# Performance work log

Hardware: AMD Instinct MI355X
Metric: run time of the kernel (lower is better)

The kernel has to match this reference:

```python
import jax, jax.numpy as jnp
import numpy as np

B, S, H = 16, 8192, 512

def setup_inputs() -> dict:
    key = jax.random.key(0)
    k1, k2, k3, k4, k5 = jax.random.split(key, 5)
    scale = 1.0 / np.sqrt(H)
    return {
        "encoder_outputs": jax.random.normal(k1, (B, S, H), dtype=jnp.float32),
        "query": jax.random.normal(k2, (B, H), dtype=jnp.float32),
        "W_h": jax.random.normal(k3, (H, H), dtype=jnp.float32) * scale,
        "W_q": jax.random.normal(k4, (H, H), dtype=jnp.float32) * scale,
        "v": jax.random.normal(k5, (H,), dtype=jnp.float32) * scale,
    }

def reference(encoder_outputs, query, W_h, W_q, v):
    # h_proj: (B,S,H) = enc @ W_h^T (torch Linear convention)
    h_proj = jnp.einsum('bsh,oh->bso', encoder_outputs, W_h)
    # q_proj: (B,1,H)
    q_proj = jnp.einsum('bh,oh->bo', query, W_q)[:, None, :]
    # scores: (B,S) = tanh(h_proj + q_proj) @ v
    scores = jnp.einsum('bso,o->bs', jnp.tanh(h_proj + q_proj), v)
    alpha = jax.nn.softmax(scores, axis=1)          # (B,S)
    context = jnp.einsum('bs,bsh->bh', alpha, encoder_outputs)  # (B,H)
    return (context, alpha)
```

## Files before the change

kernel.cpp:

```cpp
#include <hip/hip_runtime.h>

typedef float  f32x4  __attribute__((ext_vector_type(4)));
typedef __bf16 bf16x8 __attribute__((ext_vector_type(8)));

#define LOG2E      1.4426950408889634f
#define TWO_LOG2E  2.8853900817779268f

__device__ __forceinline__ float fast_tanh(float x) {
    float e = __builtin_amdgcn_exp2f(x * TWO_LOG2E);
    return 1.0f - 2.0f * __builtin_amdgcn_rcpf(e + 1.0f);
}

__device__ __forceinline__ int a_chunk(int m, int k8) {
    return (((m >> 4) * 16 + (k8 >> 2)) << 6) +
           ((((k8 & 3) << 4) | (m & 15)) ^ ((k8 >> 2) & 7) ^ (((k8 & 3) << 1) & 7));
}

__global__ void wh_swizzle_kernel(const float* __restrict__ Wh,
                                  __bf16* __restrict__ Wswz) {
    int gid = blockIdx.x * 256 + threadIdx.x;
    int n   = gid >> 6;
    int k8  = gid & 63;
    const float* g = Wh + ((long)n << 9) + (k8 << 3);
    f32x4 f0 = *(const f32x4*)g;
    f32x4 f1 = *(const f32x4*)(g + 4);
    bf16x8 val;
    val[0] = (__bf16)f0[0]; val[1] = (__bf16)f0[1];
    val[2] = (__bf16)f0[2]; val[3] = (__bf16)f0[3];
    val[4] = (__bf16)f1[0]; val[5] = (__bf16)f1[1];
    val[6] = (__bf16)f1[2]; val[7] = (__bf16)f1[3];
    int chunk = (((n >> 4) * 16 + (k8 >> 2)) << 6) + (((k8 & 3) << 4) | (n & 15));
    *(bf16x8*)(Wswz + ((long)chunk << 3)) = val;
}

__global__ void qproj_kernel(const float* __restrict__ query,
                             const float* __restrict__ Wq,
                             float* __restrict__ qp) {
    int pair = (blockIdx.x << 2) + (threadIdx.x >> 6);
    int l    = threadIdx.x & 63;
    int b    = pair >> 9;
    long o   = pair & 511;
    const f32x4* q  = (const f32x4*)(query + (b << 9) + (l << 3));
    const f32x4* wr = (const f32x4*)(Wq + (o << 9) + (l << 3));
    f32x4 a0 = q[0], a1 = q[1], w0 = wr[0], w1 = wr[1];
    float acc = a0[0]*w0[0] + a0[1]*w0[1] + a0[2]*w0[2] + a0[3]*w0[3]
              + a1[0]*w1[0] + a1[1]*w1[1] + a1[2]*w1[2] + a1[3]*w1[3];
    #pragma unroll
    for (int off = 1; off < 64; off <<= 1) acc += __shfl_xor(acc, off, 64);
    if (l == 0) qp[pair] = acc;
}

__global__ __launch_bounds__(512, 4) void score_ctx_kernel(
    const float*  __restrict__ enc,
    const __bf16* __restrict__ Wswz,
    const float*  __restrict__ qp,
    const float*  __restrict__ v,
    float* __restrict__ alpha_out,
    float* __restrict__ ctx_acc,
    float* __restrict__ denom)
{
    __shared__ __align__(16) unsigned char ldsA[65536];
    __shared__ float score_lds[512];
    __shared__ float escore[64];

    const int  t    = threadIdx.x;
    const int  w    = t >> 6;
    const int  l    = t & 63;
    const long row0 = (long)blockIdx.x << 6;
    const int  b    = (int)(row0 >> 13);

    f32x4 acc[4][4];
    float vv[4];
    #pragma unroll
    for (int nt = 0; nt < 4; ++nt) {
        int n = (w << 6) + (nt << 4) + (l & 15);
        float q = qp[(b << 9) + n];
        vv[nt] = v[n];
        f32x4 qv = {q, q, q, q};
        #pragma unroll
        for (int mt = 0; mt < 4; ++mt) acc[nt][mt] = qv;
    }

    #pragma unroll
    for (int i = 0; i < 8; ++i) {
        int cflat = t + (i << 9);
        int m = cflat >> 6, k8 = cflat & 63;
        const float* g = enc + ((row0 + m) << 9) + (k8 << 3);
        f32x4 f0 = *(const f32x4*)g;
        f32x4 f1 = *(const f32x4*)(g + 4);
        bf16x8 val;
        val[0] = (__bf16)f0[0]; val[1] = (__bf16)f0[1];
        val[2] = (__bf16)f0[2]; val[3] = (__bf16)f0[3];
        val[4] = (__bf16)f1[0]; val[5] = (__bf16)f1[1];
        val[6] = (__bf16)f1[2]; val[7] = (__bf16)f1[3];
        *(bf16x8*)(ldsA + (a_chunk(m, k8) << 4)) = val;
    }

    __syncthreads();

    const bf16x8* Bg = (const bf16x8*)Wswz;
    #pragma unroll 2
    for (int s = 0; s < 16; ++s) {
        bf16x8 af[4];
        int lowr = l ^ (s & 7) ^ (((l >> 4) << 1) & 7);
        #pragma unroll
        for (int mt = 0; mt < 4; ++mt)
            af[mt] = *(const bf16x8*)(ldsA + (((((mt << 4) + s) << 6) + lowr) << 4));
        #pragma unroll
        for (int nt = 0; nt < 4; ++nt) {
            bf16x8 bf = Bg[((((w << 2) + nt) * 16 + s) << 6) + l];
            #pragma unroll
            for (int mt = 0; mt < 4; ++mt)
                acc[nt][mt] = __builtin_amdgcn_mfma_f32_16x16x32_bf16(
                    af[mt], bf, acc[nt][mt], 0, 0, 0);
        }
    }

    float srow[16];
    #pragma unroll
    for (int i = 0; i < 16; ++i) srow[i] = 0.f;
    #pragma unroll
    for (int nt = 0; nt < 4; ++nt) {
        float vn = vv[nt];
        #pragma unroll
        for (int mt = 0; mt < 4; ++mt)
            #pragma unroll
            for (int r = 0; r < 4; ++r)
                srow[mt * 4 + r] += vn * fast_tanh(acc[nt][mt][r]);
    }
    #pragma unroll
    for (int i = 0; i < 16; ++i) {
        #pragma unroll
        for (int off = 1; off < 16; off <<= 1)
            srow[i] += __shfl_xor(srow[i], off, 64);
    }
    if ((l & 15) == 0) {
        int qd = l >> 4;
        #pragma unroll
        for (int mt = 0; mt < 4; ++mt)
            #pragma unroll
            for (int r = 0; r < 4; ++r)
                score_lds[(w << 6) + (mt << 4) + (qd << 2) + r] = srow[mt * 4 + r];
    }
    __syncthreads();

    if (t < 64) {
        float sc = 0.f;
        #pragma unroll
        for (int ww = 0; ww < 8; ++ww) sc += score_lds[(ww << 6) + t];
        float e = __builtin_amdgcn_exp2f(sc * LOG2E);
        alpha_out[row0 + t] = e;
        escore[t] = e;
        float ssum = e;
        #pragma unroll
        for (int off = 1; off < 64; off <<= 1) ssum += __shfl_xor(ssum, off, 64);
        if (t == 0) atomicAdd(denom + b, ssum);
    }
    __syncthreads();

    float ca[8];
    #pragma unroll
    for (int j = 0; j < 8; ++j) ca[j] = 0.f;
    #pragma unroll
    for (int ii = 0; ii < 8; ++ii) {
        int m = (w << 3) + ii;
        float em = escore[m];
        bf16x8 av = *(const bf16x8*)(ldsA + (a_chunk(m, l) << 4));
        #pragma unroll
        for (int j = 0; j < 8; ++j) ca[j] += em * (float)av[j];
    }
    __syncthreads();
    float* part = (float*)ldsA;
    #pragma unroll
    for (int j = 0; j < 8; ++j) part[t * 9 + j] = ca[j];
    __syncthreads();
    {
        int h = t;
        int k8h = h >> 3, j = h & 7;
        float sum = 0.f;
        #pragma unroll
        for (int rg = 0; rg < 8; ++rg) sum += part[((rg << 6) | k8h) * 9 + j];
        atomicAdd(ctx_acc + ((long)b << 9) + h, sum);
    }
}

__global__ void normalize_kernel(const float* __restrict__ ctx_acc,
                                 const float* __restrict__ denom,
                                 float* __restrict__ out) {
    int i = blockIdx.x * 256 + threadIdx.x;
    if (i < 8192) {
        int b = i >> 9;
        out[i] = ctx_acc[i] / denom[b];
    } else if (i < 8192 + 131072) {
        int b = (i - 8192) >> 13;
        out[i] = out[i] / denom[b];
    }
}

extern "C" void kernel_launch(void* const* d_in, const int* in_sizes, int n_in,
                              void* d_out, int out_size, void* d_ws, size_t ws_size,
                              hipStream_t stream) {
    const float* enc   = (const float*)d_in[0];
    const float* query = (const float*)d_in[1];
    const float* Wh    = (const float*)d_in[2];
    const float* Wq    = (const float*)d_in[3];
    const float* v     = (const float*)d_in[4];
    float* out = (float*)d_out;

    char* ws = (char*)d_ws;
    float*  ctx_acc = (float*)ws;
    float*  denom   = (float*)(ws + 32768);
    float*  qp      = (float*)(ws + 32832);
    __bf16* Wswz    = (__bf16*)(ws + 65600);

    hipMemsetAsync(ws, 0, 32832, stream);
    wh_swizzle_kernel<<<128, 256, 0, stream>>>(Wh, Wswz);
    qproj_kernel<<<2048, 256, 0, stream>>>(query, Wq, qp);
    score_ctx_kernel<<<2048, 512, 0, stream>>>(enc, Wswz, qp, v,
                                               out + 8192, ctx_acc, denom);
    normalize_kernel<<<544, 256, 0, stream>>>(ctx_acc, denom, out);
}
```

Baseline: 424.2 us.

## Merge prolog kernels, double the block size, and software-pipeline MFMA operand loads

The memset, Wh swizzle and q-projection launches are folded into a single prolog kernel, removing two launches. The score kernel now uses 1024 threads, so each wave covers 32 output columns instead of 64, which halves the accumulator registers. The K loop is software-pipelined: the next LDS A fragments and the B fragments two steps ahead are loaded while the current MFMAs run. The context partial sums gain an extra LDS reduction pass. With launch_bounds(1024,4) and 64KB of LDS per block, fewer blocks can be resident and register pressure is tighter.

```diff
diff --git a/kernel.cpp b/kernel.cpp
--- a/kernel.cpp
+++ b/kernel.cpp
@@ -16,41 +16,50 @@
            ((((k8 & 3) << 4) | (m & 15)) ^ ((k8 >> 2) & 7) ^ (((k8 & 3) << 1) & 7));
 }
 
-__global__ void wh_swizzle_kernel(const float* __restrict__ Wh,
-                                  __bf16* __restrict__ Wswz) {
-    int gid = blockIdx.x * 256 + threadIdx.x;
-    int n   = gid >> 6;
-    int k8  = gid & 63;
-    const float* g = Wh + ((long)n << 9) + (k8 << 3);
-    f32x4 f0 = *(const f32x4*)g;
-    f32x4 f1 = *(const f32x4*)(g + 4);
-    bf16x8 val;
-    val[0] = (__bf16)f0[0]; val[1] = (__bf16)f0[1];
-    val[2] = (__bf16)f0[2]; val[3] = (__bf16)f0[3];
-    val[4] = (__bf16)f1[0]; val[5] = (__bf16)f1[1];
-    val[6] = (__bf16)f1[2]; val[7] = (__bf16)f1[3];
-    int chunk = (((n >> 4) * 16 + (k8 >> 2)) << 6) + (((k8 & 3) << 4) | (n & 15));
-    *(bf16x8*)(Wswz + ((long)chunk << 3)) = val;
-}
-
-__global__ void qproj_kernel(const float* __restrict__ query,
-                             const float* __restrict__ Wq,
-                             float* __restrict__ qp) {
-    int pair = (blockIdx.x << 2) + (threadIdx.x >> 6);
-    int l    = threadIdx.x & 63;
-    int b    = pair >> 9;
-    long o   = pair & 511;
-    const f32x4* q  = (const f32x4*)(query + (b << 9) + (l << 3));
-    const f32x4* wr = (const f32x4*)(Wq + (o << 9) + (l << 3));
-    f32x4 a0 = q[0], a1 = q[1], w0 = wr[0], w1 = wr[1];
-    float acc = a0[0]*w0[0] + a0[1]*w0[1] + a0[2]*w0[2] + a0[3]*w0[3]
-              + a1[0]*w1[0] + a1[1]*w1[1] + a1[2]*w1[2] + a1[3]*w1[3];
-    #pragma unroll
-    for (int off = 1; off < 64; off <<= 1) acc += __shfl_xor(acc, off, 64);
-    if (l == 0) qp[pair] = acc;
-}
-
-__global__ __launch_bounds__(512, 4) void score_ctx_kernel(
+__global__ void prolog_kernel(const float* __restrict__ Wh,
+                              __bf16* __restrict__ Wswz,
+                              const float* __restrict__ query,
+                              const float* __restrict__ Wq,
+                              float* __restrict__ qp,
+                              float* __restrict__ ctx_acc,
+                              float* __restrict__ denom) {
+    const int bid = blockIdx.x;
+    const int t   = threadIdx.x;
+    if (bid < 128) {
+        int gid = (bid << 8) + t;
+        int n   = gid >> 6;
+        int k8  = gid & 63;
+        const float* g = Wh + ((long)n << 9) + (k8 << 3);
+        f32x4 f0 = *(const f32x4*)g;
+        f32x4 f1 = *(const f32x4*)(g + 4);
+        bf16x8 val;
+        val[0] = (__bf16)f0[0]; val[1] = (__bf16)f0[1];
+        val[2] = (__bf16)f0[2]; val[3] = (__bf16)f0[3];
+        val[4] = (__bf16)f1[0]; val[5] = (__bf16)f1[1];
+        val[6] = (__bf16)f1[2]; val[7] = (__bf16)f1[3];
+        int chunk = (((n >> 4) * 16 + (k8 >> 2)) << 6) + (((k8 & 3) << 4) | (n & 15));
+        *(bf16x8*)(Wswz + ((long)chunk << 3)) = val;
+    } else if (bid < 2176) {
+        int pair = ((bid - 128) << 2) + (t >> 6);
+        int l    = t & 63;
+        int b    = pair >> 9;
+        long o   = pair & 511;
+        const f32x4* q  = (const f32x4*)(query + (b << 9) + (l << 3));
+        const f32x4* wr = (const f32x4*)(Wq + (o << 9) + (l << 3));
+        f32x4 a0 = q[0], a1 = q[1], w0 = wr[0], w1 = wr[1];
+        float acc = a0[0]*w0[0] + a0[1]*w0[1] + a0[2]*w0[2] + a0[3]*w0[3]
+                  + a1[0]*w1[0] + a1[1]*w1[1] + a1[2]*w1[2] + a1[3]*w1[3];
+        #pragma unroll
+        for (int off = 1; off < 64; off <<= 1) acc += __shfl_xor(acc, off, 64);
+        if (l == 0) qp[pair] = acc;
+    } else {
+        int i = ((bid - 2176) << 8) + t;
+        if (i < 8192)      ctx_acc[i] = 0.f;
+        else if (i < 8208) denom[i - 8192] = 0.f;
+    }
+}
+
+__global__ __launch_bounds__(1024, 4) void score_ctx_kernel(
     const float*  __restrict__ enc,
     const __bf16* __restrict__ Wswz,
     const float*  __restrict__ qp,
@@ -60,7 +69,7 @@
     float* __restrict__ denom)
 {
     __shared__ __align__(16) unsigned char ldsA[65536];
-    __shared__ float score_lds[512];
+    __shared__ float score_lds[1024];
     __shared__ float escore[64];
 
     const int  t    = threadIdx.x;
@@ -69,11 +78,11 @@
     const long row0 = (long)blockIdx.x << 6;
     const int  b    = (int)(row0 >> 13);
 
-    f32x4 acc[4][4];
-    float vv[4];
-    #pragma unroll
-    for (int nt = 0; nt < 4; ++nt) {
-        int n = (w << 6) + (nt << 4) + (l & 15);
+    f32x4 acc[2][4];
+    float vv[2];
+    #pragma unroll
+    for (int nt = 0; nt < 2; ++nt) {
+        int n = (w << 5) + (nt << 4) + (l & 15);
         float q = qp[(b << 9) + n];
         vv[nt] = v[n];
         f32x4 qv = {q, q, q, q};
@@ -82,9 +91,9 @@
     }
 
     #pragma unroll
-    for (int i = 0; i < 8; ++i) {
-        int cflat = t + (i << 9);
-        int m = cflat >> 6, k8 = cflat & 63;
+    for (int i = 0; i < 4; ++i) {
+        int m  = (t >> 6) + (i << 4);
+        int k8 = t & 63;
         const float* g = enc + ((row0 + m) << 9) + (k8 << 3);
         f32x4 f0 = *(const f32x4*)g;
         f32x4 f1 = *(const f32x4*)(g + 4);
@@ -96,23 +105,44 @@
         *(bf16x8*)(ldsA + (a_chunk(m, k8) << 4)) = val;
     }
 
-    __syncthreads();
-
     const bf16x8* Bg = (const bf16x8*)Wswz;
-    #pragma unroll 2
+    const int j0 = w << 1;
+    bf16x8 bfr[2][2];
+    #pragma unroll
+    for (int nt = 0; nt < 2; ++nt) {
+        bfr[0][nt] = Bg[(((j0 + nt) << 4) + 0 << 6) + l];
+        bfr[1][nt] = Bg[((((j0 + nt) << 4) + 1) << 6) + l];
+    }
+
+    __syncthreads();
+
+    bf16x8 af[2][4];
+    {
+        int lowr = l ^ 0 ^ (((l >> 4) << 1) & 7);
+        #pragma unroll
+        for (int mt = 0; mt < 4; ++mt)
+            af[0][mt] = *(const bf16x8*)(ldsA + ((((mt << 4) << 6) + lowr) << 4));
+    }
+    #pragma unroll
     for (int s = 0; s < 16; ++s) {
-        bf16x8 af[4];
-        int lowr = l ^ (s & 7) ^ (((l >> 4) << 1) & 7);
-        #pragma unroll
-        for (int mt = 0; mt < 4; ++mt)
-            af[mt] = *(const bf16x8*)(ldsA + (((((mt << 4) + s) << 6) + lowr) << 4));
-        #pragma unroll
-        for (int nt = 0; nt < 4; ++nt) {
-            bf16x8 bf = Bg[((((w << 2) + nt) * 16 + s) << 6) + l];
+        const int cur = s & 1, nxt = cur ^ 1;
+        if (s < 15) {
+            int lowr = l ^ ((s + 1) & 7) ^ (((l >> 4) << 1) & 7);
+            #pragma unroll
+            for (int mt = 0; mt < 4; ++mt)
+                af[nxt][mt] = *(const bf16x8*)(
+                    ldsA + (((((mt << 4) + s + 1) << 6) + lowr) << 4));
+        }
+        #pragma unroll
+        for (int nt = 0; nt < 2; ++nt)
             #pragma unroll
             for (int mt = 0; mt < 4; ++mt)
                 acc[nt][mt] = __builtin_amdgcn_mfma_f32_16x16x32_bf16(
-                    af[mt], bf, acc[nt][mt], 0, 0, 0);
+                    af[cur][mt], bfr[cur][nt], acc[nt][mt], 0, 0, 0);
+        if (s + 2 < 16) {
+            #pragma unroll
+            for (int nt = 0; nt < 2; ++nt)
+                bfr[cur][nt] = Bg[((((j0 + nt) << 4) + s + 2) << 6) + l];
         }
     }
 
@@ -120,7 +150,7 @@
     #pragma unroll
     for (int i = 0; i < 16; ++i) srow[i] = 0.f;
     #pragma unroll
-    for (int nt = 0; nt < 4; ++nt) {
+    for (int nt = 0; nt < 2; ++nt) {
         float vn = vv[nt];
         #pragma unroll
         for (int mt = 0; mt < 4; ++mt)
@@ -147,7 +177,7 @@
     if (t < 64) {
         float sc = 0.f;
         #pragma unroll
-        for (int ww = 0; ww < 8; ++ww) sc += score_lds[(ww << 6) + t];
+        for (int ww = 0; ww < 16; ++ww) sc += score_lds[(ww << 6) + t];
         float e = __builtin_amdgcn_exp2f(sc * LOG2E);
         alpha_out[row0 + t] = e;
         escore[t] = e;
@@ -162,8 +192,8 @@
     #pragma unroll
     for (int j = 0; j < 8; ++j) ca[j] = 0.f;
     #pragma unroll
-    for (int ii = 0; ii < 8; ++ii) {
-        int m = (w << 3) + ii;
+    for (int ii = 0; ii < 4; ++ii) {
+        int m = (w << 2) + ii;
         float em = escore[m];
         bf16x8 av = *(const bf16x8*)(ldsA + (a_chunk(m, l) << 4));
         #pragma unroll
@@ -171,10 +201,18 @@
     }
     __syncthreads();
     float* part = (float*)ldsA;
-    #pragma unroll
-    for (int j = 0; j < 8; ++j) part[t * 9 + j] = ca[j];
-    __syncthreads();
-    {
+    if (t < 512) {
+        #pragma unroll
+        for (int j = 0; j < 8; ++j) part[t * 9 + j] = ca[j];
+    }
+    __syncthreads();
+    if (t >= 512) {
+        int p = t - 512;
+        #pragma unroll
+        for (int j = 0; j < 8; ++j) part[p * 9 + j] += ca[j];
+    }
+    __syncthreads();
+    if (t < 512) {
         int h = t;
         int k8h = h >> 3, j = h & 7;
         float sum = 0.f;
@@ -213,10 +251,9 @@
     float*  qp      = (float*)(ws + 32832);
     __bf16* Wswz    = (__bf16*)(ws + 65600);
 
-    hipMemsetAsync(ws, 0, 32832, stream);
-    wh_swizzle_kernel<<<128, 256, 0, stream>>>(Wh, Wswz);
-    qproj_kernel<<<2048, 256, 0, stream>>>(query, Wq, qp);
-    score_ctx_kernel<<<2048, 512, 0, stream>>>(enc, Wswz, qp, v,
-                                               out + 8192, ctx_acc, denom);
+    prolog_kernel<<<2209, 256, 0, stream>>>(Wh, Wswz, query, Wq, qp,
+                                            ctx_acc, denom);
+    score_ctx_kernel<<<2048, 1024, 0, stream>>>(enc, Wswz, qp, v,
+                                                out + 8192, ctx_acc, denom);
     normalize_kernel<<<544, 256, 0, stream>>>(ctx_acc, denom, out);
 }
```

Measured after the change: 445.5 us. +5.0%, slower.
